# Optimization experiments

Measured on AMD Instinct MI355X. Metric: run time of the kernel, lower is better.

The kernel has to match this reference:

```python
import jax, jax.numpy as jnp
import numpy as np

B, IN, H = 4096, 1024, 1024


def setup_inputs() -> dict:
    key = jax.random.key(0)
    ks = jax.random.split(key, 20)
    s_in = 1.0 / np.sqrt(IN)
    s_h = 1.0 / np.sqrt(H)
    def lin(kw, kb, fan_in, scale):
        W = jax.random.uniform(kw, (H, fan_in), jnp.float32, -scale, scale)
        b = jax.random.uniform(kb, (H,), jnp.float32, -scale, scale)
        return W, b
    Wxf, bxf = lin(ks[0], ks[1], IN, s_in)
    Whf, bhf = lin(ks[2], ks[3], H, s_h)
    Wxi, bxi = lin(ks[4], ks[5], IN, s_in)
    Whi, bhi = lin(ks[6], ks[7], H, s_h)
    Wxo, bxo = lin(ks[8], ks[9], IN, s_in)
    Who, bho = lin(ks[10], ks[11], H, s_h)
    Wxc, bxc = lin(ks[12], ks[13], IN, s_in)
    Whc, bhc = lin(ks[14], ks[15], H, s_h)
    x = jax.random.normal(ks[16], (B, IN), jnp.float32)
    c = jax.random.normal(ks[17], (B, H), jnp.float32)
    h = jax.random.normal(ks[18], (B, H), jnp.float32)
    return dict(x=x, c=c, h=h,
                Wxf=Wxf, bxf=bxf, Whf=Whf, bhf=bhf,
                Wxi=Wxi, bxi=bxi, Whi=Whi, bhi=bhi,
                Wxo=Wxo, bxo=bxo, Who=Who, bho=bho,
                Wxc=Wxc, bxc=bxc, Whc=Whc, bhc=bhc)


def reference(x, c, h,
              Wxf, bxf, Whf, bhf,
              Wxi, bxi, Whi, bhi,
              Wxo, bxo, Who, bho,
              Wxc, bxc, Whc, bhc):
    # Fuse the 8 small GEMMs into two batched GEMMs: x @ Wx^T and h @ Wh^T
    # with gate outputs concatenated along the hidden dim [f, i, o, c~].
    Wx = jnp.concatenate([Wxf, Wxi, Wxo, Wxc], axis=0)   # [4H, IN]
    Wh = jnp.concatenate([Whf, Whi, Who, Whc], axis=0)   # [4H, H]
    bx = jnp.concatenate([bxf, bxi, bxo, bxc], axis=0)   # [4H]
    bh = jnp.concatenate([bhf, bhi, bho, bhc], axis=0)   # [4H]
    gates = x @ Wx.T + h @ Wh.T + (bx + bh)              # [B, 4H]
    hs = Wxf.shape[0]
    f = jax.nn.sigmoid(gates[:, 0 * hs:1 * hs])
    i = jax.nn.sigmoid(gates[:, 1 * hs:2 * hs])
    o = jax.nn.sigmoid(gates[:, 2 * hs:3 * hs])
    ctil = jnp.tanh(gates[:, 3 * hs:4 * hs])
    ct = f * c + ctil * i
    ht = jnp.tanh(ct) * o
    return (ct, ht)
```

## Files before the change

### kernel.cpp

```cpp
#include <hip/hip_runtime.h>
#include <hip/hip_bf16.h>
#include <stdint.h>

typedef __hip_bfloat16 bf16;
typedef __attribute__((ext_vector_type(8))) short short8;
typedef __attribute__((ext_vector_type(4))) float floatx4;

#define AS1(p) ((const __attribute__((address_space(1))) void*)(p))
#define AS3(p) ((__attribute__((address_space(3))) void*)(p))

#define M_DIM 4096
#define H_DIM 1024
#define MEG   (1u << 20)

__device__ __forceinline__ unsigned short f2bf(float f) {
    uint32_t u = __float_as_uint(f);
    uint32_t r = (u + 0x7FFFu + ((u >> 16) & 1u)) >> 16;
    return (unsigned short)r;
}

__device__ __forceinline__ float fast_sigmoid(float v) {
    return 1.0f / (1.0f + __expf(-v));
}
__device__ __forceinline__ float fast_tanh(float v) {
    return 2.0f / (1.0f + __expf(-2.0f * v)) - 1.0f;
}

__global__ __launch_bounds__(256)
void convert_to_bf16(const float* __restrict__ x, const float* __restrict__ h,
                     const float* Wxf, const float* Wxi, const float* Wxo, const float* Wxc,
                     const float* Whf, const float* Whi, const float* Who, const float* Whc,
                     unsigned short* __restrict__ ws)
{
    const uint32_t idx0 = blockIdx.x * 2048u + threadIdx.x * 8u;
    const uint32_t t = blockIdx.x >> 9;
    const float* src;
    uint32_t off;
    if (t < 4u)      { src = x; off = idx0; }
    else if (t < 8u) { src = h; off = idx0 - (4u << 20); }
    else {
        const uint32_t g = t - 8u;
        src = (g == 0) ? Wxf : (g == 1) ? Wxi : (g == 2) ? Wxo : (g == 3) ? Wxc
            : (g == 4) ? Whf : (g == 5) ? Whi : (g == 6) ? Who : Whc;
        off = idx0 & (MEG - 1u);
    }
    const float4 v0 = *(const float4*)(src + off);
    const float4 v1 = *(const float4*)(src + off + 4);
    short8 pk;
    pk[0] = (short)f2bf(v0.x); pk[1] = (short)f2bf(v0.y);
    pk[2] = (short)f2bf(v0.z); pk[3] = (short)f2bf(v0.w);
    pk[4] = (short)f2bf(v1.x); pk[5] = (short)f2bf(v1.y);
    pk[6] = (short)f2bf(v1.z); pk[7] = (short)f2bf(v1.w);
    *(short8*)(ws + idx0) = pk;
}

__global__ __launch_bounds__(256, 2)
void lstm_fused_kernel(const unsigned short* __restrict__ ws,
                       const float* __restrict__ c,
                       const float* __restrict__ bxf, const float* __restrict__ bhf,
                       const float* __restrict__ bxi, const float* __restrict__ bhi,
                       const float* __restrict__ bxo, const float* __restrict__ bho,
                       const float* __restrict__ bxc, const float* __restrict__ bhc,
                       float* __restrict__ out)
{
    __shared__ __align__(16) char lds[24576];
    const bf16* ldsA = (const bf16*)lds;
    const bf16* ldsB = (const bf16*)(lds + 8192);

    const int tid  = threadIdx.x;
    const int w    = tid >> 6;
    const int lane = tid & 63;

    const int bm0 = blockIdx.x * 128;
    const int bn0 = blockIdx.y * 64;

    const unsigned short* srcP0[6];
    const unsigned short* srcP1[6];
    uint32_t goff[6];
    uint32_t loff[6];
#pragma unroll
    for (int i = 0; i < 6; ++i) {
        const int ch = w * 6 + i;
        if (ch < 8) {
            const int row = bm0 + ch * 16 + (lane >> 2);
            srcP0[i] = ws;
            srcP1[i] = ws + (4u << 20);
            goff[i] = (uint32_t)row * 1024u + (uint32_t)(lane & 3) * 8u;
            loff[i] = (uint32_t)ch * 1024u;
        } else {
            const int b = ch - 8;
            const int g = b >> 2;
            const int n = bn0 + (b & 3) * 16 + (lane >> 2);
            srcP0[i] = ws + (8u << 20)  + (uint32_t)g * MEG;
            srcP1[i] = ws + (12u << 20) + (uint32_t)g * MEG;
            goff[i] = (uint32_t)n * 1024u + (uint32_t)(lane & 3) * 8u;
            loff[i] = 8192u + (uint32_t)b * 1024u;
        }
    }

    const int wrow  = (w & 1) * 64;
    const int wcol  = (w >> 1) * 32;
    const int lrc   = lane & 15;
    const int lquad = lane >> 4;

    uint32_t aoff[4];
#pragma unroll
    for (int mt = 0; mt < 4; ++mt)
        aoff[mt] = (uint32_t)((wrow + mt * 16 + lrc) * 32 + lquad * 8);
    uint32_t boff[4][2];
#pragma unroll
    for (int g = 0; g < 4; ++g)
#pragma unroll
        for (int nt = 0; nt < 2; ++nt)
            boff[g][nt] = (uint32_t)(g * 2048 + (wcol + nt * 16 + lrc) * 32 + lquad * 8);

    floatx4 acc[4][4][2];
#pragma unroll
    for (int g = 0; g < 4; ++g)
#pragma unroll
        for (int mt = 0; mt < 4; ++mt)
#pragma unroll
            for (int nt = 0; nt < 2; ++nt)
                acc[g][mt][nt] = (floatx4){0.f, 0.f, 0.f, 0.f};

    for (int kt = 0; kt < 64; ++kt) {
        const int phase = kt >> 5;
        const uint32_t k0 = (uint32_t)(kt & 31) * 32u;
#pragma unroll
        for (int i = 0; i < 6; ++i) {
            const unsigned short* src = phase ? srcP1[i] : srcP0[i];
            __builtin_amdgcn_global_load_lds(AS1(src + goff[i] + k0),
                                             AS3(lds + loff[i]), 16, 0, 0);
        }
        asm volatile("s_waitcnt vmcnt(0)" ::: "memory");
        __syncthreads();

        short8 afr[4];
#pragma unroll
        for (int mt = 0; mt < 4; ++mt)
            afr[mt] = *(const short8*)(ldsA + aoff[mt]);
#pragma unroll
        for (int g = 0; g < 4; ++g) {
#pragma unroll
            for (int nt = 0; nt < 2; ++nt) {
                const short8 bfr = *(const short8*)(ldsB + boff[g][nt]);
#pragma unroll
                for (int mt = 0; mt < 4; ++mt)
                    acc[g][mt][nt] = __builtin_amdgcn_mfma_f32_16x16x32_bf16(
                        afr[mt], bfr, acc[g][mt][nt], 0, 0, 0);
            }
        }
        __syncthreads();
    }

    float* out_ct = out;
    float* out_ht = out + (size_t)M_DIM * H_DIM;
#pragma unroll
    for (int nt = 0; nt < 2; ++nt) {
        const int col = bn0 + wcol + nt * 16 + lrc;
        const float bf_ = bxf[col] + bhf[col];
        const float bi_ = bxi[col] + bhi[col];
        const float bo_ = bxo[col] + bho[col];
        const float bc_ = bxc[col] + bhc[col];
#pragma unroll
        for (int mt = 0; mt < 4; ++mt) {
#pragma unroll
            for (int r = 0; r < 4; ++r) {
                const int row = bm0 + wrow + mt * 16 + lquad * 4 + r;
                const float gf = acc[0][mt][nt][r] + bf_;
                const float gi = acc[1][mt][nt][r] + bi_;
                const float go = acc[2][mt][nt][r] + bo_;
                const float gc = acc[3][mt][nt][r] + bc_;
                const float f    = fast_sigmoid(gf);
                const float ii   = fast_sigmoid(gi);
                const float o    = fast_sigmoid(go);
                const float ctil = fast_tanh(gc);
                const float cv   = c[(size_t)row * H_DIM + col];
                const float ctn  = f * cv + ctil * ii;
                const float htn  = fast_tanh(ctn) * o;
                out_ct[(size_t)row * H_DIM + col] = ctn;
                out_ht[(size_t)row * H_DIM + col] = htn;
            }
        }
    }
}

extern "C" void kernel_launch(void* const* d_in, const int* in_sizes, int n_in,
                              void* d_out, int out_size, void* d_ws, size_t ws_size,
                              hipStream_t stream) {
    (void)in_sizes; (void)n_in; (void)out_size; (void)ws_size;
    const float* x   = (const float*)d_in[0];
    const float* c   = (const float*)d_in[1];
    const float* h   = (const float*)d_in[2];
    const float* Wxf = (const float*)d_in[3];  const float* bxf = (const float*)d_in[4];
    const float* Whf = (const float*)d_in[5];  const float* bhf = (const float*)d_in[6];
    const float* Wxi = (const float*)d_in[7];  const float* bxi = (const float*)d_in[8];
    const float* Whi = (const float*)d_in[9];  const float* bhi = (const float*)d_in[10];
    const float* Wxo = (const float*)d_in[11]; const float* bxo = (const float*)d_in[12];
    const float* Who = (const float*)d_in[13]; const float* bho = (const float*)d_in[14];
    const float* Wxc = (const float*)d_in[15]; const float* bxc = (const float*)d_in[16];
    const float* Whc = (const float*)d_in[17]; const float* bhc = (const float*)d_in[18];
    float* out = (float*)d_out;
    unsigned short* ws = (unsigned short*)d_ws;

    convert_to_bf16<<<8192, 256, 0, stream>>>(x, h,
        Wxf, Wxi, Wxo, Wxc, Whf, Whi, Who, Whc, ws);

    dim3 grid(M_DIM / 128, H_DIM / 64);
    lstm_fused_kernel<<<grid, 256, 0, stream>>>(ws, c,
        bxf, bhf, bxi, bhi, bxo, bho, bxc, bhc, out);
}
```

Measured before the change: 232.0 us.

## Double-buffer LDS tiles with async prefetch and XOR-swizzle LDS layout

Doubles the LDS tile buffer so global-to-LDS loads for the next K step are issued before computing the current one, using vmcnt-based waits and raw barriers instead of full drains. It also XOR-swizzles the 16-byte chunk placement within each row, on both the load and the fragment-read side, to reduce LDS bank conflicts. LDS use rises to 48KB per block, which may limit occupancy with two blocks per CU, and the hand-written waitcnt and barrier sequence is fragile.

```diff
diff --git a/kernel.cpp b/kernel.cpp
--- a/kernel.cpp
+++ b/kernel.cpp
@@ -12,6 +12,7 @@
 #define M_DIM 4096
 #define H_DIM 1024
 #define MEG   (1u << 20)
+#define LDS_BUF 24576
 
 __device__ __forceinline__ unsigned short f2bf(float f) {
     uint32_t u = __float_as_uint(f);
@@ -63,9 +64,7 @@
                        const float* __restrict__ bxc, const float* __restrict__ bhc,
                        float* __restrict__ out)
 {
-    __shared__ __align__(16) char lds[24576];
-    const bf16* ldsA = (const bf16*)lds;
-    const bf16* ldsB = (const bf16*)(lds + 8192);
+    __shared__ __align__(16) char lds[2 * LDS_BUF];
 
     const int tid  = threadIdx.x;
     const int w    = tid >> 6;
@@ -74,6 +73,7 @@
     const int bm0 = blockIdx.x * 128;
     const int bn0 = blockIdx.y * 64;
 
+    const uint32_t cg = (((uint32_t)lane & 3u) ^ (((uint32_t)lane >> 3) & 3u)) * 8u;
     const unsigned short* srcP0[6];
     const unsigned short* srcP1[6];
     uint32_t goff[6];
@@ -85,7 +85,7 @@
             const int row = bm0 + ch * 16 + (lane >> 2);
             srcP0[i] = ws;
             srcP1[i] = ws + (4u << 20);
-            goff[i] = (uint32_t)row * 1024u + (uint32_t)(lane & 3) * 8u;
+            goff[i] = (uint32_t)row * 1024u + cg;
             loff[i] = (uint32_t)ch * 1024u;
         } else {
             const int b = ch - 8;
@@ -93,7 +93,7 @@
             const int n = bn0 + (b & 3) * 16 + (lane >> 2);
             srcP0[i] = ws + (8u << 20)  + (uint32_t)g * MEG;
             srcP1[i] = ws + (12u << 20) + (uint32_t)g * MEG;
-            goff[i] = (uint32_t)n * 1024u + (uint32_t)(lane & 3) * 8u;
+            goff[i] = (uint32_t)n * 1024u + cg;
             loff[i] = 8192u + (uint32_t)b * 1024u;
         }
     }
@@ -103,16 +103,18 @@
     const int lrc   = lane & 15;
     const int lquad = lane >> 4;
 
+    const uint32_t kslot = (((uint32_t)lquad ^ (((uint32_t)lrc >> 1) & 3u))) * 8u;
+
     uint32_t aoff[4];
 #pragma unroll
     for (int mt = 0; mt < 4; ++mt)
-        aoff[mt] = (uint32_t)((wrow + mt * 16 + lrc) * 32 + lquad * 8);
+        aoff[mt] = (uint32_t)((wrow + mt * 16 + lrc) * 32) + kslot;
     uint32_t boff[4][2];
 #pragma unroll
     for (int g = 0; g < 4; ++g)
 #pragma unroll
         for (int nt = 0; nt < 2; ++nt)
-            boff[g][nt] = (uint32_t)(g * 2048 + (wcol + nt * 16 + lrc) * 32 + lquad * 8);
+            boff[g][nt] = (uint32_t)(g * 2048 + (wcol + nt * 16 + lrc) * 32) + kslot;
 
     floatx4 acc[4][4][2];
 #pragma unroll
@@ -123,35 +125,49 @@
             for (int nt = 0; nt < 2; ++nt)
                 acc[g][mt][nt] = (floatx4){0.f, 0.f, 0.f, 0.f};
 
-    for (int kt = 0; kt < 64; ++kt) {
+    auto issue_loads = [&](int kt) {
         const int phase = kt >> 5;
         const uint32_t k0 = (uint32_t)(kt & 31) * 32u;
+        const uint32_t bb = (uint32_t)(kt & 1) * LDS_BUF;
 #pragma unroll
         for (int i = 0; i < 6; ++i) {
             const unsigned short* src = phase ? srcP1[i] : srcP0[i];
             __builtin_amdgcn_global_load_lds(AS1(src + goff[i] + k0),
-                                             AS3(lds + loff[i]), 16, 0, 0);
-        }
-        asm volatile("s_waitcnt vmcnt(0)" ::: "memory");
-        __syncthreads();
-
+                                             AS3(lds + bb + loff[i]), 16, 0, 0);
+        }
+    };
+    auto compute = [&](int kt) {
+        const char* base = lds + (uint32_t)(kt & 1) * LDS_BUF;
+        const bf16* lA = (const bf16*)base;
+        const bf16* lB = (const bf16*)(base + 8192);
         short8 afr[4];
 #pragma unroll
         for (int mt = 0; mt < 4; ++mt)
-            afr[mt] = *(const short8*)(ldsA + aoff[mt]);
+            afr[mt] = *(const short8*)(lA + aoff[mt]);
 #pragma unroll
         for (int g = 0; g < 4; ++g) {
 #pragma unroll
             for (int nt = 0; nt < 2; ++nt) {
-                const short8 bfr = *(const short8*)(ldsB + boff[g][nt]);
+                const short8 bfr = *(const short8*)(lB + boff[g][nt]);
 #pragma unroll
                 for (int mt = 0; mt < 4; ++mt)
                     acc[g][mt][nt] = __builtin_amdgcn_mfma_f32_16x16x32_bf16(
                         afr[mt], bfr, acc[g][mt][nt], 0, 0, 0);
             }
         }
-        __syncthreads();
-    }
+    };
+
+    issue_loads(0);
+    asm volatile("s_waitcnt vmcnt(0)\ns_barrier" ::: "memory");
+
+    for (int kt = 0; kt < 63; ++kt) {
+        issue_loads(kt + 1);
+        asm volatile("s_waitcnt vmcnt(6)\ns_barrier" ::: "memory");
+        compute(kt);
+        asm volatile("s_waitcnt lgkmcnt(0)\ns_barrier" ::: "memory");
+    }
+    asm volatile("s_waitcnt vmcnt(0)\ns_barrier" ::: "memory");
+    compute(63);
 
     float* out_ct = out;
     float* out_ht = out + (size_t)M_DIM * H_DIM;
```

Result: faster. 222.9 us (-3.9%).
